# Optimization experiments

Measured on AMD Instinct MI355X. Metric: run time of the kernel, lower is better.

## Reference

```python
import jax, jax.numpy as jnp
import numpy as np

B, D, N = 32768, 128, 8
TEMP = 0.25          # episodic_memory_temperature
DECAY = 0.99         # episodic_strength_decay
AGE_INC = 0.02       # episodic_age_increment


def _l2norm(x, eps=1e-6):
    n = jnp.sqrt(jnp.sum(x * x, axis=-1, keepdims=True))
    return x / jnp.maximum(n, eps)


def setup_inputs() -> dict:
    key = jax.random.key(0)
    ks = jax.random.split(key, 16)
    s = 0.05
    inp = {
        'signal': jax.random.normal(ks[0], (B, D), jnp.float32),
        'previous': jax.random.normal(ks[1], (B, D), jnp.float32),
        'hidden': jax.random.normal(ks[2], (B, D), jnp.float32),
        'episodic_keys': jax.random.normal(ks[3], (B, N, D), jnp.float32),
        'episodic_values': jax.random.normal(ks[4], (B, N, D), jnp.float32),
        'episodic_strength': jax.random.uniform(ks[5], (B, N), jnp.float32),
        'episodic_age': jax.random.uniform(ks[6], (B, N), jnp.float32),
        # Linear weights stored as [in, out] (torch stores [out, in]); small random
        # instead of the zero init so gradients flow for kernel testing.
        'w_read_query': jax.random.normal(ks[7], (2 * D, D), jnp.float32) * s,
        'w_read_mix': jax.random.normal(ks[8], (2 * D, 1), jnp.float32) * s,
        'b_read_mix': jnp.full((1,), -0.2, jnp.float32),
        'w_key': jax.random.normal(ks[9], (2 * D, D), jnp.float32) * s,
        'b_key': jnp.zeros((D,), jnp.float32),
        'w_value': jax.random.normal(ks[10], (2 * D, D), jnp.float32) * s,
        'b_value': jnp.zeros((D,), jnp.float32),
        'w_write': jax.random.normal(ks[11], (2 * D, 1), jnp.float32) * s,
        'b_write': jnp.full((1,), -0.6, jnp.float32),
        'w_persist': jax.random.normal(ks[12], (2 * D, 1), jnp.float32) * s,
        'b_persist': jnp.zeros((1,), jnp.float32),
        'w_merge': jax.random.normal(ks[13], (2 * D, 1), jnp.float32) * s,
        'b_merge': jnp.zeros((1,), jnp.float32),
    }
    return inp


def reference(signal, previous, hidden, episodic_keys, episodic_values,
              episodic_strength, episodic_age,
              w_read_query, w_read_mix, b_read_mix, w_key, b_key, w_value,
              b_value, w_write, b_write, w_persist, b_persist, w_merge, b_merge):
    dtype = signal.dtype
    n_slots = episodic_keys.shape[1]

    # ---------------- read ----------------
    sp = jnp.concatenate([signal, previous], axis=-1)             # [B, 2D]
    query = _l2norm(sp @ w_read_query)                            # [B, D]
    norm_keys = _l2norm(episodic_keys)                            # [B, N, D]
    content_scores = jnp.einsum('bd,bnd->bn', query, norm_keys)   # [B, N]
    content_w = jax.nn.softmax(content_scores / TEMP, axis=-1)
    content_read = jnp.einsum('bn,bnd->bd', content_w, episodic_values)
    persistent_scores = 2.4 * episodic_strength + 0.6 * (1.0 - episodic_age)
    persistent_w = jax.nn.softmax(persistent_scores / TEMP, axis=-1)
    persistent_read = jnp.einsum('bn,bnd->bd', persistent_w, episodic_values)
    read_mix = jax.nn.sigmoid(sp @ w_read_mix + b_read_mix)       # [B, 1]
    memory_read = read_mix * content_read + (1.0 - read_mix) * persistent_read

    # ---------------- write ----------------
    joined = jnp.concatenate([signal, hidden], axis=-1)           # [B, 2D]
    candidate_key = jnp.tanh(joined @ w_key + b_key)              # [B, D]
    candidate_value = jnp.tanh(joined @ w_value + b_value)        # [B, D]
    write_strength = jax.nn.sigmoid(joined @ w_write + b_write)   # [B, 1]
    persistence = jax.nn.sigmoid(joined @ w_persist + b_persist)  # [B, 1]
    similarity = jnp.einsum('bd,bnd->bn', _l2norm(candidate_key), norm_keys)

    top_k = min(3, n_slots)
    top_sim, top_idx = jax.lax.top_k(similarity, top_k)           # [B, 3]
    max_sim = top_sim[:, 0]
    merge_index = top_idx[:, 0]
    second_sim = top_sim[:, 1]
    novelty = jnp.clip(1.0 - max_sim, 0.0, 1.0)[:, None]          # [B, 1]

    replace_scores = (1.2 * episodic_age + 1.0 * (1.0 - episodic_strength)
                      + 0.5 * (1.0 - similarity))
    replace_index = jnp.argmax(replace_scores, axis=-1)
    merge_pref = jax.nn.sigmoid(joined @ w_merge + b_merge + 2.6 * max_sim[:, None])

    full_m = (max_sim > 0.78) & (merge_pref[:, 0] >= 0.55)
    multi_m = full_m & (second_sim > 0.68)
    partial_m = (~multi_m) & (max_sim > 0.64) & (second_sim > 0.52)

    rows = jnp.arange(signal.shape[0])[:, None]
    target_w = jax.nn.one_hot(replace_index, n_slots, dtype=dtype)
    partial_w = jax.nn.softmax(top_sim[:, :2] / TEMP, axis=-1)
    partial_target = jnp.zeros_like(target_w).at[rows, top_idx[:, :2]].add(partial_w)
    multi_w = jax.nn.softmax(top_sim / TEMP, axis=-1)
    multi_target = jnp.zeros_like(target_w).at[rows, top_idx].add(multi_w)
    full_target = jax.nn.one_hot(merge_index, n_slots, dtype=dtype)

    target_w = jnp.where(full_m[:, None], full_target, target_w)
    target_w = jnp.where(partial_m[:, None], partial_target, target_w)
    target_w = jnp.where(multi_m[:, None], multi_target, target_w)

    scale = jnp.where(multi_m[:, None], 0.16 + 0.52 * write_strength,
                      jnp.where(partial_m[:, None], 0.18 + 0.62 * write_strength,
                                0.20 + 0.80 * write_strength))
    overwrite = target_w * scale * (0.55 + 0.45 * novelty)        # [B, N]
    ow3 = overwrite[..., None]                                    # [B, N, 1]

    merge_like = full_m | partial_m | multi_m
    key_mix = jnp.where(merge_like[:, None], 0.28 + 0.24 * persistence,
                        0.78 + 0.16 * persistence)[:, :, None]    # [B, 1, 1]
    value_mix = jnp.where(merge_like[:, None], 0.42 + 0.28 * persistence,
                          0.82 + 0.12 * persistence)[:, :, None]

    updated_keys = episodic_keys + ow3 * key_mix * (candidate_key[:, None, :] - episodic_keys)
    updated_values = episodic_values + ow3 * value_mix * (candidate_value[:, None, :] - episodic_values)

    boost = overwrite * (0.45 + 0.35 * persistence + 0.45 * novelty + 0.25 * write_strength)
    updated_strength = jnp.clip(episodic_strength * DECAY + boost, 0.0, 1.0)
    updated_age = jnp.clip((episodic_age + AGE_INC) * (1.0 - overwrite), 0.0, 1.0)

    return memory_read, updated_keys, updated_values, updated_strength, updated_age
```

## Files before the change

kernel.cpp:

```cpp
#include <hip/hip_runtime.h>
#include <cstddef>

#define BD 128
#define NS 8
#define ROWS 8
#define BLOCK 256

typedef float __attribute__((ext_vector_type(2))) f32x2;

__device__ __forceinline__ float sigm(float x) { return 1.0f / (1.0f + __expf(-x)); }

__device__ __forceinline__ void nt_store2(float2 v, float2* p) {
    f32x2 t; t.x = v.x; t.y = v.y;
    __builtin_nontemporal_store(t, (f32x2*)p);
}

__global__ __launch_bounds__(BLOCK, 4)
void sbcore_kernel(
    const float* __restrict__ g_signal, const float* __restrict__ g_prev,
    const float* __restrict__ g_hidden, const float* __restrict__ g_keys,
    const float* __restrict__ g_vals, const float* __restrict__ g_str,
    const float* __restrict__ g_age,
    const float* __restrict__ w_rq, const float* __restrict__ w_mix,
    const float* __restrict__ b_mix, const float* __restrict__ w_key,
    const float* __restrict__ b_key, const float* __restrict__ w_val,
    const float* __restrict__ b_val, const float* __restrict__ w_wr,
    const float* __restrict__ b_wr, const float* __restrict__ w_pe,
    const float* __restrict__ b_pe, const float* __restrict__ w_mg,
    const float* __restrict__ b_mg,
    float* __restrict__ o_read, float* __restrict__ o_keys,
    float* __restrict__ o_vals, float* __restrict__ o_str,
    float* __restrict__ o_age)
{
    __shared__ __align__(16) float sig_s[ROWS][BD];
    __shared__ __align__(16) float prv_s[ROWS][BD];
    __shared__ __align__(16) float hid_s[ROWS][BD];
    __shared__ __align__(16) float wmix_s[2*BD], wwr_s[2*BD], wpe_s[2*BD], wmg_s[2*BD];
    __shared__ __align__(16) float str_s[ROWS*NS], age_s[ROWS*NS];
    __shared__ float red_s[4][4][2];
    __shared__ float ckinv_s[ROWS];
    __shared__ __align__(16) float head_s[ROWS][4];

    const int tid = threadIdx.x;
    const int row0 = blockIdx.x * ROWS;

    for (int i = tid; i < ROWS*BD; i += BLOCK) {
        int r = i >> 7, dd = i & (BD-1);
        size_t g = (size_t)(row0 + r) * BD + dd;
        sig_s[r][dd] = g_signal[g];
        prv_s[r][dd] = g_prev[g];
        hid_s[r][dd] = g_hidden[g];
    }
    if (tid < ROWS*NS) {
        str_s[tid] = g_str[(size_t)row0*NS + tid];
        age_s[tid] = g_age[(size_t)row0*NS + tid];
    }
    wmix_s[tid] = w_mix[tid];
    wwr_s[tid]  = w_wr[tid];
    wpe_s[tid]  = w_pe[tid];
    wmg_s[tid]  = w_mg[tid];
    __syncthreads();

    {
        const int dotid = tid >> 3;
        const int hr    = dotid >> 2;
        const int hh    = dotid & 3;
        const int hj    = tid & 7;
        const float* ws = (hh==0) ? wmix_s : (hh==1) ? wwr_s : (hh==2) ? wpe_s : wmg_s;
        const float* xb;
        if (hj < 4) xb = &sig_s[hr][0];
        else        xb = ((hh==0) ? &prv_s[hr][0] : &hid_s[hr][0]) - BD;
        float p = 0.f;
#pragma unroll
        for (int q = 0; q < 8; ++q) {
            const int k = hj*32 + q*4;
            const float4 w4 = *(const float4*)&ws[k];
            const float4 x4 = *(const float4*)&xb[k];
            p = fmaf(x4.w, w4.w, fmaf(x4.z, w4.z, fmaf(x4.y, w4.y, fmaf(x4.x, w4.x, p))));
        }
        p += __shfl_xor(p, 1); p += __shfl_xor(p, 2); p += __shfl_xor(p, 4);
        if (hj == 0) head_s[hr][hh] = p;
    }

    const int d    = tid & (BD-1);
    const int h    = tid >> 7;
    const int wave = tid >> 6;
    const int lane = tid & 63;

    float aq[4], ak[4], av[4];
#pragma unroll
    for (int r = 0; r < 4; ++r) { aq[r] = 0.f; ak[r] = 0.f; av[r] = 0.f; }

    for (int kk = 0; kk < BD; kk += 4) {
        float wq0 = w_rq[(kk+0)*BD + d], wq1 = w_rq[(kk+1)*BD + d],
              wq2 = w_rq[(kk+2)*BD + d], wq3 = w_rq[(kk+3)*BD + d];
        float wk0 = w_key[(kk+0)*BD + d], wk1 = w_key[(kk+1)*BD + d],
              wk2 = w_key[(kk+2)*BD + d], wk3 = w_key[(kk+3)*BD + d];
        float wv0 = w_val[(kk+0)*BD + d], wv1 = w_val[(kk+1)*BD + d],
              wv2 = w_val[(kk+2)*BD + d], wv3 = w_val[(kk+3)*BD + d];
#pragma unroll
        for (int r = 0; r < 4; ++r) {
            const float4 s4 = *(const float4*)&sig_s[h*4 + r][kk];
            aq[r] = fmaf(s4.w, wq3, fmaf(s4.z, wq2, fmaf(s4.y, wq1, fmaf(s4.x, wq0, aq[r]))));
            ak[r] = fmaf(s4.w, wk3, fmaf(s4.z, wk2, fmaf(s4.y, wk1, fmaf(s4.x, wk0, ak[r]))));
            av[r] = fmaf(s4.w, wv3, fmaf(s4.z, wv2, fmaf(s4.y, wv1, fmaf(s4.x, wv0, av[r]))));
        }
    }
    for (int kk = 0; kk < BD; kk += 4) {
        const int k = kk + BD;
        float wq0 = w_rq[(k+0)*BD + d], wq1 = w_rq[(k+1)*BD + d],
              wq2 = w_rq[(k+2)*BD + d], wq3 = w_rq[(k+3)*BD + d];
        float wk0 = w_key[(k+0)*BD + d], wk1 = w_key[(k+1)*BD + d],
              wk2 = w_key[(k+2)*BD + d], wk3 = w_key[(k+3)*BD + d];
        float wv0 = w_val[(k+0)*BD + d], wv1 = w_val[(k+1)*BD + d],
              wv2 = w_val[(k+2)*BD + d], wv3 = w_val[(k+3)*BD + d];
#pragma unroll
        for (int r = 0; r < 4; ++r) {
            const float4 p4 = *(const float4*)&prv_s[h*4 + r][kk];
            const float4 h4 = *(const float4*)&hid_s[h*4 + r][kk];
            aq[r] = fmaf(p4.w, wq3, fmaf(p4.z, wq2, fmaf(p4.y, wq1, fmaf(p4.x, wq0, aq[r]))));
            ak[r] = fmaf(h4.w, wk3, fmaf(h4.z, wk2, fmaf(h4.y, wk1, fmaf(h4.x, wk0, ak[r]))));
            av[r] = fmaf(h4.w, wv3, fmaf(h4.z, wv2, fmaf(h4.y, wv1, fmaf(h4.x, wv0, av[r]))));
        }
    }

    const float bk = b_key[d], bv = b_val[d];
    float ckr[4], cvr[4], q2[4], c2[4];
#pragma unroll
    for (int r = 0; r < 4; ++r) {
        ckr[r] = tanhf(ak[r] + bk);
        cvr[r] = tanhf(av[r] + bv);
        q2[r]  = aq[r] * aq[r];
        c2[r]  = ckr[r] * ckr[r];
    }
#pragma unroll
    for (int off = 32; off > 0; off >>= 1) {
#pragma unroll
        for (int r = 0; r < 4; ++r) {
            q2[r] += __shfl_xor(q2[r], off);
            c2[r] += __shfl_xor(c2[r], off);
        }
    }
    if (lane == 0) {
#pragma unroll
        for (int r = 0; r < 4; ++r) { red_s[wave][r][0] = q2[r]; red_s[wave][r][1] = c2[r]; }
    }
    __syncthreads();
#pragma unroll
    for (int r = 0; r < 4; ++r) {
        float sq = red_s[h*2][r][0] + red_s[h*2+1][r][0];
        float sc = red_s[h*2][r][1] + red_s[h*2+1][r][1];
        float qi = 1.0f / fmaxf(sqrtf(sq), 1e-6f);
        sig_s[h*4 + r][d] = aq[r] * qi;
        prv_s[h*4 + r][d] = ckr[r];
        hid_s[h*4 + r][d] = cvr[r];
        if (d == 0) ckinv_s[h*4 + r] = 1.0f / fmaxf(sqrtf(sc), 1e-6f);
    }
    __syncthreads();

    const float bmix = b_mix[0], bwr = b_wr[0], bpe = b_pe[0], bmg = b_mg[0];
    const int sj = lane & 7;

    for (int rr = 0; rr < 2; ++rr) {
        const int r = wave*2 + rr;
        const size_t row = (size_t)row0 + r;
        const size_t kvb = row * (size_t)(NS*BD);

        const float4* kp4  = (const float4*)(g_keys + kvb);
        const float4* qrow = (const float4*)&sig_s[r][0];
        const float4* crow = (const float4*)&prv_s[r][0];
        float pk = 0.f, pq = 0.f, pc = 0.f;
#pragma unroll
        for (int q = 0; q < 4; ++q) {
            const float4 k4 = kp4[4*lane + q];
            const float4 q4 = qrow[sj*4 + q];
            const float4 c4 = crow[sj*4 + q];
            pk = fmaf(k4.w,k4.w, fmaf(k4.z,k4.z, fmaf(k4.y,k4.y, fmaf(k4.x,k4.x, pk))));
            pq = fmaf(q4.w,k4.w, fmaf(q4.z,k4.z, fmaf(q4.y,k4.y, fmaf(q4.x,k4.x, pq))));
            pc = fmaf(c4.w,k4.w, fmaf(c4.z,k4.z, fmaf(c4.y,k4.y, fmaf(c4.x,k4.x, pc))));
        }
        const float2* vp = (const float2*)(g_vals + kvb);
        float2 vf[NS];
#pragma unroll
        for (int n = 0; n < NS; ++n) vf[n] = vp[n*64 + lane];
        const float2 cki = *(const float2*)&prv_s[r][2*lane];
        const float2 cvi = *(const float2*)&hid_s[r][2*lane];

        pk += __shfl_xor(pk, 1); pk += __shfl_xor(pk, 2); pk += __shfl_xor(pk, 4);
        pq += __shfl_xor(pq, 1); pq += __shfl_xor(pq, 2); pq += __shfl_xor(pq, 4);
        pc += __shfl_xor(pc, 1); pc += __shfl_xor(pc, 2); pc += __shfl_xor(pc, 4);
        const float ki   = 1.0f / fmaxf(sqrtf(pk), 1e-6f);
        const float csn  = pq * ki;
        const float simn = pc * ki * ckinv_s[r];
        float cs[NS], sim[NS];
#pragma unroll
        for (int m = 0; m < NS; ++m) {
            cs[m]  = __shfl(csn,  m*8);
            sim[m] = __shfl(simn, m*8);
        }

        const float4 hd = *(const float4*)&head_s[r][0];
        const float mix   = sigm(hd.x + bmix);
        const float wsv   = sigm(hd.y + bwr);
        const float pev   = sigm(hd.z + bpe);
        const float mglin = hd.w + bmg;

        float mC = cs[0];
#pragma unroll
        for (int n = 1; n < NS; ++n) mC = fmaxf(mC, cs[n]);
        float eC[NS], sC = 0.f;
#pragma unroll
        for (int n = 0; n < NS; ++n) { eC[n] = __expf((cs[n]-mC)*4.0f); sC += eC[n]; }
        const float4 st0 = *(const float4*)&str_s[r*NS];
        const float4 st1 = *(const float4*)&str_s[r*NS+4];
        const float4 ag0 = *(const float4*)&age_s[r*NS];
        const float4 ag1 = *(const float4*)&age_s[r*NS+4];
        const float stv[NS] = {st0.x,st0.y,st0.z,st0.w,st1.x,st1.y,st1.z,st1.w};
        const float agv[NS] = {ag0.x,ag0.y,ag0.z,ag0.w,ag1.x,ag1.y,ag1.z,ag1.w};
        float psc[NS]; float mP = -1e30f;
#pragma unroll
        for (int n = 0; n < NS; ++n) {
            psc[n] = fmaf(2.4f, stv[n], 0.6f*(1.0f - agv[n]));
            mP = fmaxf(mP, psc[n]);
        }
        float eP[NS], sP = 0.f;
#pragma unroll
        for (int n = 0; n < NS; ++n) { eP[n] = __expf((psc[n]-mP)*4.0f); sP += eP[n]; }
        const float icS = 1.0f/sC, ipS = 1.0f/sP;

        float2 cr = make_float2(0.f, 0.f), prd = make_float2(0.f, 0.f);
#pragma unroll
        for (int n = 0; n < NS; ++n) {
            float wc = eC[n]*icS, wp = eP[n]*ipS;
            cr.x  = fmaf(wc, vf[n].x, cr.x);  cr.y  = fmaf(wc, vf[n].y, cr.y);
            prd.x = fmaf(wp, vf[n].x, prd.x); prd.y = fmaf(wp, vf[n].y, prd.y);
        }
        float2 mr;
        mr.x = mix*cr.x + (1.0f-mix)*prd.x;
        mr.y = mix*cr.y + (1.0f-mix)*prd.y;
        nt_store2(mr, &((float2*)(o_read + row*BD))[lane]);

        float tv0 = -1e30f; int ti0 = 0;
#pragma unroll
        for (int n = 0; n < NS; ++n) if (sim[n] > tv0) { tv0 = sim[n]; ti0 = n; }
        float tv1 = -1e30f; int ti1 = 0;
#pragma unroll
        for (int n = 0; n < NS; ++n) {
            float v = (n == ti0) ? -1e30f : sim[n];
            if (v > tv1) { tv1 = v; ti1 = n; }
        }
        float tv2 = -1e30f; int ti2 = 0;
#pragma unroll
        for (int n = 0; n < NS; ++n) {
            float v = (n == ti0 || n == ti1) ? -1e30f : sim[n];
            if (v > tv2) { tv2 = v; ti2 = n; }
        }

        float rm = -1e30f; int ri = 0;
#pragma unroll
        for (int n = 0; n < NS; ++n) {
            float rsv = fmaf(1.2f, agv[n], (1.0f - stv[n])) + 0.5f*(1.0f - sim[n]);
            if (rsv > rm) { rm = rsv; ri = n; }
        }

        const float mpref = sigm(mglin + 2.6f*tv0);
        const bool full  = (tv0 > 0.78f) && (mpref >= 0.55f);
        const bool multi = full && (tv1 > 0.68f);
        const bool part  = (!multi) && (tv0 > 0.64f) && (tv1 > 0.52f);
        const float nov  = fminf(fmaxf(1.0f - tv0, 0.0f), 1.0f);

        float a0, a1, a2, aR;
        if (multi) {
            float e1 = __expf((tv1 - tv0)*4.0f), e2 = __expf((tv2 - tv0)*4.0f);
            float inv = 1.0f/(1.0f + e1 + e2);
            a0 = inv; a1 = e1*inv; a2 = e2*inv; aR = 0.f;
        } else if (part) {
            float e1 = __expf((tv1 - tv0)*4.0f);
            float inv = 1.0f/(1.0f + e1);
            a0 = inv; a1 = e1*inv; a2 = 0.f; aR = 0.f;
        } else if (full) {
            a0 = 1.f; a1 = 0.f; a2 = 0.f; aR = 0.f;
        } else {
            a0 = 0.f; a1 = 0.f; a2 = 0.f; aR = 1.f;
        }

        const float scl = multi ? fmaf(0.52f, wsv, 0.16f)
                        : part  ? fmaf(0.62f, wsv, 0.18f)
                                : fmaf(0.80f, wsv, 0.20f);
        const bool  mlike = full || part || multi;
        const float km  = mlike ? fmaf(0.24f, pev, 0.28f) : fmaf(0.16f, pev, 0.78f);
        const float vm  = mlike ? fmaf(0.28f, pev, 0.42f) : fmaf(0.12f, pev, 0.82f);
        const float owc = scl * fmaf(0.45f, nov, 0.55f);
        const float bco = 0.45f + 0.35f*pev + 0.45f*nov + 0.25f*wsv;

        const float2* kp2 = (const float2*)(g_keys + kvb);
        float2* okp = (float2*)(o_keys + kvb);
        float2* ovp = (float2*)(o_vals + kvb);
#pragma unroll
        for (int n = 0; n < NS; ++n) {
            const float2 kf2 = kp2[n*64 + lane];
            float tn = ((n==ti0) ? a0 : (n==ti1) ? a1 : (n==ti2) ? a2 : 0.f)
                     + ((n==ri) ? aR : 0.f);
            float ow = tn*owc;
            float a = ow*km, b2 = ow*vm;
            float2 uk, uv;
            uk.x = fmaf(a,  cki.x - kf2.x, kf2.x);
            uk.y = fmaf(a,  cki.y - kf2.y, kf2.y);
            uv.x = fmaf(b2, cvi.x - vf[n].x, vf[n].x);
            uv.y = fmaf(b2, cvi.y - vf[n].y, vf[n].y);
            nt_store2(uk, &okp[n*64 + lane]);
            nt_store2(uv, &ovp[n*64 + lane]);
        }
        if (lane < NS) {
            float tn = ((lane==ti0) ? a0 : (lane==ti1) ? a1 : (lane==ti2) ? a2 : 0.f)
                     + ((lane==ri) ? aR : 0.f);
            float ow = tn*owc;
            float us = fminf(fmaxf(fmaf(str_s[r*NS+lane], 0.99f, ow*bco), 0.f), 1.f);
            float ua = fminf(fmaxf((age_s[r*NS+lane] + 0.02f)*(1.0f - ow), 0.f), 1.f);
            o_str[row*NS + lane] = us;
            o_age[row*NS + lane] = ua;
        }
    }
}

extern "C" void kernel_launch(void* const* d_in, const int* in_sizes, int n_in,
                              void* d_out, int out_size, void* d_ws, size_t ws_size,
                              hipStream_t stream) {
    const float* g_signal = (const float*)d_in[0];
    const float* g_prev   = (const float*)d_in[1];
    const float* g_hidden = (const float*)d_in[2];
    const float* g_keys   = (const float*)d_in[3];
    const float* g_vals   = (const float*)d_in[4];
    const float* g_str    = (const float*)d_in[5];
    const float* g_age    = (const float*)d_in[6];
    const float* w_rq     = (const float*)d_in[7];
    const float* w_mix    = (const float*)d_in[8];
    const float* b_mix    = (const float*)d_in[9];
    const float* w_key    = (const float*)d_in[10];
    const float* b_key    = (const float*)d_in[11];
    const float* w_val    = (const float*)d_in[12];
    const float* b_val    = (const float*)d_in[13];
    const float* w_wr     = (const float*)d_in[14];
    const float* b_wr     = (const float*)d_in[15];
    const float* w_pe     = (const float*)d_in[16];
    const float* b_pe     = (const float*)d_in[17];
    const float* w_mg     = (const float*)d_in[18];
    const float* b_mg     = (const float*)d_in[19];

    const size_t B = (size_t)in_sizes[0] / BD;
    float* out   = (float*)d_out;
    float* o_read = out;
    float* o_keys = o_read + B*BD;
    float* o_vals = o_keys + B*NS*BD;
    float* o_str  = o_vals + B*NS*BD;
    float* o_age  = o_str  + B*NS;

    const int blocks = (int)(B / ROWS);
    sbcore_kernel<<<dim3(blocks), dim3(BLOCK), 0, stream>>>(
        g_signal, g_prev, g_hidden, g_keys, g_vals, g_str, g_age,
        w_rq, w_mix, b_mix, w_key, b_key, w_val, b_val,
        w_wr, b_wr, w_pe, b_pe, w_mg, b_mg,
        o_read, o_keys, o_vals, o_str, o_age);
}
```

Measured before the change: 634.3 us.

## Process 32 rows per block to amortize projection weight loads

Raises rows per block from 8 to 32, so each thread accumulates 16 rows of the query/key/value projections for every weight value it loads from global memory. The weight traffic per row drops about fourfold. Input staging now uses float4 loads, and the four scalar head dot products read their weights straight from global memory instead of staging them in LDS. The trade-off is much higher register pressure (48 accumulators plus 64 temporaries per thread), a lowered launch-bounds occupancy hint of 3, larger LDS use, and a quarter as many blocks.

Result: slower. 651.1 us (+2.7%).

```diff
diff --git a/kernel.cpp b/kernel.cpp
--- a/kernel.cpp
+++ b/kernel.cpp
@@ -3,7 +3,7 @@
 
 #define BD 128
 #define NS 8
-#define ROWS 8
+#define ROWS 32
 #define BLOCK 256
 
 typedef float __attribute__((ext_vector_type(2))) f32x2;
@@ -15,7 +15,7 @@
     __builtin_nontemporal_store(t, (f32x2*)p);
 }
 
-__global__ __launch_bounds__(BLOCK, 4)
+__global__ __launch_bounds__(BLOCK, 3)
 void sbcore_kernel(
     const float* __restrict__ g_signal, const float* __restrict__ g_prev,
     const float* __restrict__ g_hidden, const float* __restrict__ g_keys,
@@ -35,50 +35,48 @@
     __shared__ __align__(16) float sig_s[ROWS][BD];
     __shared__ __align__(16) float prv_s[ROWS][BD];
     __shared__ __align__(16) float hid_s[ROWS][BD];
-    __shared__ __align__(16) float wmix_s[2*BD], wwr_s[2*BD], wpe_s[2*BD], wmg_s[2*BD];
     __shared__ __align__(16) float str_s[ROWS*NS], age_s[ROWS*NS];
-    __shared__ float red_s[4][4][2];
+    __shared__ float red_s[4][16][2];
     __shared__ float ckinv_s[ROWS];
     __shared__ __align__(16) float head_s[ROWS][4];
 
     const int tid = threadIdx.x;
     const int row0 = blockIdx.x * ROWS;
 
-    for (int i = tid; i < ROWS*BD; i += BLOCK) {
-        int r = i >> 7, dd = i & (BD-1);
-        size_t g = (size_t)(row0 + r) * BD + dd;
-        sig_s[r][dd] = g_signal[g];
-        prv_s[r][dd] = g_prev[g];
-        hid_s[r][dd] = g_hidden[g];
-    }
-    if (tid < ROWS*NS) {
-        str_s[tid] = g_str[(size_t)row0*NS + tid];
-        age_s[tid] = g_age[(size_t)row0*NS + tid];
-    }
-    wmix_s[tid] = w_mix[tid];
-    wwr_s[tid]  = w_wr[tid];
-    wpe_s[tid]  = w_pe[tid];
-    wmg_s[tid]  = w_mg[tid];
+    {
+        const float4* gs4 = (const float4*)(g_signal + (size_t)row0 * BD);
+        const float4* gp4 = (const float4*)(g_prev   + (size_t)row0 * BD);
+        const float4* gh4 = (const float4*)(g_hidden + (size_t)row0 * BD);
+#pragma unroll
+        for (int it = 0; it < (ROWS*BD/4)/BLOCK; ++it) {
+            int i = tid + it*BLOCK;
+            int r = i >> 5, d4 = i & 31;
+            *(float4*)&sig_s[r][d4*4] = gs4[i];
+            *(float4*)&prv_s[r][d4*4] = gp4[i];
+            *(float4*)&hid_s[r][d4*4] = gh4[i];
+        }
+    }
+    str_s[tid] = g_str[(size_t)row0*NS + tid];
+    age_s[tid] = g_age[(size_t)row0*NS + tid];
     __syncthreads();
 
     {
-        const int dotid = tid >> 3;
-        const int hr    = dotid >> 2;
-        const int hh    = dotid & 3;
-        const int hj    = tid & 7;
-        const float* ws = (hh==0) ? wmix_s : (hh==1) ? wwr_s : (hh==2) ? wpe_s : wmg_s;
-        const float* xb;
-        if (hj < 4) xb = &sig_s[hr][0];
-        else        xb = ((hh==0) ? &prv_s[hr][0] : &hid_s[hr][0]) - BD;
+        const int hr = tid >> 3;
+        const int hh = (tid >> 1) & 3;
+        const int hj = tid & 1;
+        const float* ws = (hh==0) ? w_mix : (hh==1) ? w_wr : (hh==2) ? w_pe : w_mg;
+        const float4* w4p = (const float4*)(ws + hj*BD);
+        const float*  xr  = (hj==0) ? &sig_s[hr][0]
+                                    : ((hh==0) ? &prv_s[hr][0] : &hid_s[hr][0]);
+        const float4* x4p = (const float4*)xr;
         float p = 0.f;
 #pragma unroll
-        for (int q = 0; q < 8; ++q) {
-            const int k = hj*32 + q*4;
-            const float4 w4 = *(const float4*)&ws[k];
-            const float4 x4 = *(const float4*)&xb[k];
+        for (int q = 0; q < 32; ++q) {
+            const float4 w4 = w4p[q];
+            const float4 x4 = x4p[q];
             p = fmaf(x4.w, w4.w, fmaf(x4.z, w4.z, fmaf(x4.y, w4.y, fmaf(x4.x, w4.x, p))));
         }
-        p += __shfl_xor(p, 1); p += __shfl_xor(p, 2); p += __shfl_xor(p, 4);
+        p += __shfl_xor(p, 1);
         if (hj == 0) head_s[hr][hh] = p;
     }
 
@@ -87,9 +85,9 @@
     const int wave = tid >> 6;
     const int lane = tid & 63;
 
-    float aq[4], ak[4], av[4];
-#pragma unroll
-    for (int r = 0; r < 4; ++r) { aq[r] = 0.f; ak[r] = 0.f; av[r] = 0.f; }
+    float aq[16], ak[16], av[16];
+#pragma unroll
+    for (int r = 0; r < 16; ++r) { aq[r] = 0.f; ak[r] = 0.f; av[r] = 0.f; }
 
     for (int kk = 0; kk < BD; kk += 4) {
         float wq0 = w_rq[(kk+0)*BD + d], wq1 = w_rq[(kk+1)*BD + d],
@@ -99,8 +97,8 @@
         float wv0 = w_val[(kk+0)*BD + d], wv1 = w_val[(kk+1)*BD + d],
               wv2 = w_val[(kk+2)*BD + d], wv3 = w_val[(kk+3)*BD + d];
 #pragma unroll
-        for (int r = 0; r < 4; ++r) {
-            const float4 s4 = *(const float4*)&sig_s[h*4 + r][kk];
+        for (int r = 0; r < 16; ++r) {
+            const float4 s4 = *(const float4*)&sig_s[h*16 + r][kk];
             aq[r] = fmaf(s4.w, wq3, fmaf(s4.z, wq2, fmaf(s4.y, wq1, fmaf(s4.x, wq0, aq[r]))));
             ak[r] = fmaf(s4.w, wk3, fmaf(s4.z, wk2, fmaf(s4.y, wk1, fmaf(s4.x, wk0, ak[r]))));
             av[r] = fmaf(s4.w, wv3, fmaf(s4.z, wv2, fmaf(s4.y, wv1, fmaf(s4.x, wv0, av[r]))));
@@ -115,9 +113,9 @@
         float wv0 = w_val[(k+0)*BD + d], wv1 = w_val[(k+1)*BD + d],
               wv2 = w_val[(k+2)*BD + d], wv3 = w_val[(k+3)*BD + d];
 #pragma unroll
-        for (int r = 0; r < 4; ++r) {
-            const float4 p4 = *(const float4*)&prv_s[h*4 + r][kk];
-            const float4 h4 = *(const float4*)&hid_s[h*4 + r][kk];
+        for (int r = 0; r < 16; ++r) {
+            const float4 p4 = *(const float4*)&prv_s[h*16 + r][kk];
+            const float4 h4 = *(const float4*)&hid_s[h*16 + r][kk];
             aq[r] = fmaf(p4.w, wq3, fmaf(p4.z, wq2, fmaf(p4.y, wq1, fmaf(p4.x, wq0, aq[r]))));
             ak[r] = fmaf(h4.w, wk3, fmaf(h4.z, wk2, fmaf(h4.y, wk1, fmaf(h4.x, wk0, ak[r]))));
             av[r] = fmaf(h4.w, wv3, fmaf(h4.z, wv2, fmaf(h4.y, wv1, fmaf(h4.x, wv0, av[r]))));
@@ -125,9 +123,9 @@
     }
 
     const float bk = b_key[d], bv = b_val[d];
-    float ckr[4], cvr[4], q2[4], c2[4];
-#pragma unroll
-    for (int r = 0; r < 4; ++r) {
+    float ckr[16], cvr[16], q2[16], c2[16];
+#pragma unroll
+    for (int r = 0; r < 16; ++r) {
         ckr[r] = tanhf(ak[r] + bk);
         cvr[r] = tanhf(av[r] + bv);
         q2[r]  = aq[r] * aq[r];
@@ -136,33 +134,33 @@
 #pragma unroll
     for (int off = 32; off > 0; off >>= 1) {
 #pragma unroll
-        for (int r = 0; r < 4; ++r) {
+        for (int r = 0; r < 16; ++r) {
             q2[r] += __shfl_xor(q2[r], off);
             c2[r] += __shfl_xor(c2[r], off);
         }
     }
     if (lane == 0) {
 #pragma unroll
-        for (int r = 0; r < 4; ++r) { red_s[wave][r][0] = q2[r]; red_s[wave][r][1] = c2[r]; }
+        for (int r = 0; r < 16; ++r) { red_s[wave][r][0] = q2[r]; red_s[wave][r][1] = c2[r]; }
     }
     __syncthreads();
 #pragma unroll
-    for (int r = 0; r < 4; ++r) {
+    for (int r = 0; r < 16; ++r) {
         float sq = red_s[h*2][r][0] + red_s[h*2+1][r][0];
         float sc = red_s[h*2][r][1] + red_s[h*2+1][r][1];
         float qi = 1.0f / fmaxf(sqrtf(sq), 1e-6f);
-        sig_s[h*4 + r][d] = aq[r] * qi;
-        prv_s[h*4 + r][d] = ckr[r];
-        hid_s[h*4 + r][d] = cvr[r];
-        if (d == 0) ckinv_s[h*4 + r] = 1.0f / fmaxf(sqrtf(sc), 1e-6f);
+        sig_s[h*16 + r][d] = aq[r] * qi;
+        prv_s[h*16 + r][d] = ckr[r];
+        hid_s[h*16 + r][d] = cvr[r];
+        if (d == 0) ckinv_s[h*16 + r] = 1.0f / fmaxf(sqrtf(sc), 1e-6f);
     }
     __syncthreads();
 
     const float bmix = b_mix[0], bwr = b_wr[0], bpe = b_pe[0], bmg = b_mg[0];
     const int sj = lane & 7;
 
-    for (int rr = 0; rr < 2; ++rr) {
-        const int r = wave*2 + rr;
+    for (int rr = 0; rr < 8; ++rr) {
+        const int r = wave*8 + rr;
         const size_t row = (size_t)row0 + r;
         const size_t kvb = row * (size_t)(NS*BD);
 
```
